# Performance work log

Measured on AMD Instinct MI355X. Metric: run time of the kernel, lower is better.

Reference implementation:

```python
import jax, jax.numpy as jnp
import numpy as np

HEADS = 4

def _unfold3x3(x):
    # x: [N, C, H, W] -> [N, C*9, H*W], channel-slowest / kernel-fastest (matches torch F.unfold)
    N, C, H, W = x.shape
    p = jnp.pad(x, ((0, 0), (0, 0), (1, 1), (1, 1)))
    pats = jnp.stack([p[:, :, i:i + H, j:j + W] for i in range(3) for j in range(3)], axis=2)
    return pats.reshape(N, C * 9, H * W)

def _conv1x1(x, w):
    # x: [N, Cin, H, W], w: [Cout, Cin]
    return jnp.einsum('nchw,oc->nohw', x, w)

def _dwconv3x3(x, w):
    # depthwise 3x3, x: [N, C, H, W], w: [C, 1, 3, 3]
    return jax.lax.conv_general_dilated(
        x, w, window_strides=(1, 1), padding='SAME',
        feature_group_count=x.shape[1],
        dimension_numbers=('NCHW', 'OIHW', 'NCHW'))

def _layernorm(x, w, b, eps=1e-5):
    m = jnp.mean(x, axis=-1, keepdims=True)
    v = jnp.mean(jnp.square(x - m), axis=-1, keepdims=True)
    return (x - m) * jax.lax.rsqrt(v + eps) * w + b

def _l2norm(x, eps=1e-12):
    n = jnp.sqrt(jnp.sum(jnp.square(x), axis=-1, keepdims=True))
    return x / jnp.maximum(n, eps)

def setup_inputs() -> dict:
    key = jax.random.key(0)
    ks = jax.random.split(key, 12)
    channels, angRes, h, w, b = 64, 5, 32, 32, 1
    a = angRes * angRes
    D = channels * 2          # 128
    hid = int(D * 2.66)       # 340
    s = 0.02
    return {
        'buffer': jax.random.normal(ks[0], (b, channels, a, h, w), jnp.float32),
        'mlp_w': jax.random.normal(ks[1], (D, channels * 9), jnp.float32) * s,
        'ln_attn_w': jnp.ones((D,), jnp.float32),
        'ln_attn_b': jnp.zeros((D,), jnp.float32),
        'ln_ffn_w': jnp.ones((D,), jnp.float32),
        'ln_ffn_b': jnp.zeros((D,), jnp.float32),
        'qkv_w': jax.random.normal(ks[2], (3 * D, D), jnp.float32) * s,
        'qkv_dw_w': jax.random.normal(ks[3], (3 * D, 1, 3, 3), jnp.float32) * s,
        'temperature': jnp.ones((HEADS, 1, 1), jnp.float32),
        'proj_attn_w': jax.random.normal(ks[4], (D, D), jnp.float32) * s,
        'ffn_in_w': jax.random.normal(ks[5], (2 * hid, D), jnp.float32) * s,
        'ffn_dw_w': jax.random.normal(ks[6], (2 * hid, 1, 3, 3), jnp.float32) * s,
        'ffn_out_w': jax.random.normal(ks[7], (D, hid), jnp.float32) * s,
        'proj3d_w': jax.random.normal(ks[8], (channels, D), jnp.float32) * s,
    }

def reference(buffer, mlp_w, ln_attn_w, ln_attn_b, ln_ffn_w, ln_ffn_b,
              qkv_w, qkv_dw_w, temperature, proj_attn_w,
              ffn_in_w, ffn_dw_w, ffn_out_w, proj3d_w):
    b, c, a, h, w = buffer.shape
    N, D = b * a, mlp_w.shape[0]
    L = h * w
    cph = D // HEADS

    # SAI2Token: [b,c,a,h,w] -> [(b a),c,h,w] -> unfold -> [L, N, c*9] -> MLP -> [L, N, D]
    buf2d = buffer.transpose(0, 2, 1, 3, 4).reshape(N, c, h, w)
    tok = _unfold3x3(buf2d).transpose(2, 0, 1)          # [L, N, c*9]
    tok = tok @ mlp_w.T                                  # [L, N, D]

    # --- attention branch ---
    tn = _layernorm(tok, ln_attn_w, ln_attn_b)
    x = tn.transpose(1, 2, 0).reshape(N, D, h, w)        # '(h w) n d -> n d h w'
    qkv = _dwconv3x3(_conv1x1(x, qkv_w), qkv_dw_w)       # [N, 3D, h, w]
    q, k, v = jnp.split(qkv, 3, axis=1)

    def heads(t):  # 'n (head c) h w -> n head (h w) c'
        return t.reshape(N, HEADS, cph, L).transpose(0, 1, 3, 2)
    q, k, v = heads(q), heads(k), heads(v)
    q, k = _l2norm(q), _l2norm(k)
    attn = jnp.einsum('nhlc,nhmc->nhlm', q, k) * temperature  # [N, HEADS, L, L]
    attn = jax.nn.softmax(attn, axis=-1)
    out = jnp.einsum('nhlm,nhmc->nhlc', attn, v)         # [N, HEADS, L, cph]
    out = out.transpose(0, 1, 3, 2).reshape(N, D, h, w)
    out = _conv1x1(out, proj_attn_w)
    tok = tok + out.reshape(N, D, L).transpose(2, 0, 1)

    # --- GDFN branch ---
    tf = _layernorm(tok, ln_ffn_w, ln_ffn_b)
    x2 = tf.transpose(1, 2, 0).reshape(N, D, h, w)
    y = _dwconv3x3(_conv1x1(x2, ffn_in_w), ffn_dw_w)     # [N, 2*hid, h, w]
    y1, y2 = jnp.split(y, 2, axis=1)
    y = jax.nn.gelu(y1, approximate=False) * y2
    y = _conv1x1(y, ffn_out_w)                           # [N, D, h, w]
    tok = tok + y.reshape(N, D, L).transpose(2, 0, 1)

    # Token2SAI: '(h w) (b a) d -> b d a h w' then 1x1x1 conv3d
    x5 = tok.reshape(h, w, b, a, D).transpose(2, 4, 3, 0, 1)  # [b, D, a, h, w]
    out = jnp.einsum('bdahw,od->boahw', x5, proj3d_w)
    return out
```

## Files before the change

### kernel.cpp

```cpp
#include <hip/hip_runtime.h>
#include <math.h>

#define M_TOK 25600

typedef __attribute__((ext_vector_type(8))) short bf16x8;
typedef __attribute__((ext_vector_type(4))) float f32x4;
typedef __attribute__((ext_vector_type(4))) int   i32x4;
typedef __attribute__((ext_vector_type(2))) int   i32x2;

__device__ __forceinline__ unsigned short f2b(float x) {
    unsigned u = __builtin_bit_cast(unsigned, x);
    return (unsigned short)((u + 0x7fffu + ((u >> 16) & 1u)) >> 16);
}
__device__ __forceinline__ float b2f(unsigned short h) {
    unsigned u = ((unsigned)h) << 16;
    return __builtin_bit_cast(float, u);
}
__device__ __forceinline__ unsigned cvtpk(float lo, float hi) {
    unsigned r;
    asm("v_cvt_pk_bf16_f32 %0, %1, %2" : "=v"(r) : "v"(lo), "v"(hi));
    return r;
}

__global__ __launch_bounds__(256) void prep_k(const float* __restrict__ s0, const float* __restrict__ s1,
                                              const float* __restrict__ s2, const float* __restrict__ s3,
                                              const float* __restrict__ s4, const float* __restrict__ s5,
                                              const float* __restrict__ qw, const float* __restrict__ fw,
                                              short* __restrict__ dst,
                                              float* __restrict__ wqT, float* __restrict__ wgT) {
    int i = blockIdx.x * 256 + threadIdx.x;
    if (i >= 297320) return;
    if (i < 287744) {
        if (i < 81920) {
            int r = i % 640, d = i / 640;
            int tap = r >> 6, cc = r & 63;
            dst[i] = (tap < 9) ? (short)f2b(s0[(d * 64 + cc) * 9 + tap]) : (short)0;
            return;
        }
        if (i >= 234496 && i < 279552) {
            int l = i - 234496;
            int row = l / 352, col = l % 352;
            dst[i] = (col < 340) ? (short)f2b(s4[row * 340 + col]) : (short)0;
            return;
        }
        const float* s; int off;
        if      (i < 131072) { s = s1; off = i - 81920; }
        else if (i < 147456) { s = s2; off = i - 131072; }
        else if (i < 234496) { s = s3; off = i - 147456; }
        else                 { s = s5; off = i - 279552; }
        dst[i] = (short)f2b(s[off]);
        return;
    }
    int j = i - 287744;
    if (j < 3456) {
        int tap = j / 384, c = j % 384;
        wqT[j] = qw[c * 9 + tap];
    } else {
        int k = j - 3456;
        int tap = k / 680, c = k % 680;
        wgT[k] = fw[c * 9 + tap];
    }
}

template <bool ADD, bool TROUT, bool AF32>
__global__ __launch_bounds__(256) void mm64_k(const void* __restrict__ Avp,
                                              const short* __restrict__ W,
                                              float* __restrict__ outp,
                                              int M, int N, int K) {
    __shared__ __align__(16) short As[2][64 * 40];
    __shared__ __align__(16) short Bs[2][64 * 40];
    const int tid = threadIdx.x;
    const int bm = blockIdx.x * 64;
    const int bn = blockIdx.y * 64;
    const int w = tid >> 6, lane = tid & 63;
    const int h = lane >> 4, l15 = lane & 15;
    const int wm = (w >> 1) * 32, wn = (w & 1) * 32;

    const int row = tid >> 2, c4 = tid & 3;
    const int gnW = bn + row;

    f32x4 acc[2][2];
#pragma unroll
    for (int i = 0; i < 2; ++i)
#pragma unroll
        for (int j = 0; j < 2; ++j) acc[i][j] = (f32x4){0.f, 0.f, 0.f, 0.f};

    short av[8], wv[8];

    auto ldA = [&](int k0, short* tmp) {
        int gk = k0 + c4 * 8;
        size_t abase = (size_t)(bm + row) * K + gk;
        if (AF32) {
            const float* ap = (const float*)Avp + abase;
            float4 va = *(const float4*)ap;
            float4 vb = *(const float4*)(ap + 4);
            tmp[0] = (short)f2b(va.x); tmp[1] = (short)f2b(va.y);
            tmp[2] = (short)f2b(va.z); tmp[3] = (short)f2b(va.w);
            tmp[4] = (short)f2b(vb.x); tmp[5] = (short)f2b(vb.y);
            tmp[6] = (short)f2b(vb.z); tmp[7] = (short)f2b(vb.w);
        } else {
            const short* ap = (const short*)Avp + abase;
            i32x2 a = *(const i32x2*)ap;
            i32x2 b = *(const i32x2*)(ap + 4);
            *(i32x2*)&tmp[0] = a; *(i32x2*)&tmp[4] = b;
        }
    };
    auto ldW = [&](int k0, short* tmp) {
        const short* wp = W + (size_t)gnW * K + k0 + c4 * 8;
        i32x2 a = *(const i32x2*)wp;
        i32x2 b = *(const i32x2*)(wp + 4);
        *(i32x2*)&tmp[0] = a; *(i32x2*)&tmp[4] = b;
    };

    ldA(0, av);
    ldW(0, wv);

    int ph = 0;
    for (int k0 = 0; k0 < K; k0 += 32, ph ^= 1) {
        *(i32x4*)&As[ph][row * 40 + c4 * 8] = *(i32x4*)av;
        *(i32x4*)&Bs[ph][row * 40 + c4 * 8] = *(i32x4*)wv;
        if (k0 + 32 < K) {
            ldA(k0 + 32, av);
            ldW(k0 + 32, wv);
        }
        __syncthreads();

        bf16x8 af[2], bf[2];
#pragma unroll
        for (int mi = 0; mi < 2; ++mi) af[mi] = *(const bf16x8*)&As[ph][(wm + mi * 16 + l15) * 40 + h * 8];
#pragma unroll
        for (int nj = 0; nj < 2; ++nj) bf[nj] = *(const bf16x8*)&Bs[ph][(wn + nj * 16 + l15) * 40 + h * 8];
#pragma unroll
        for (int mi = 0; mi < 2; ++mi)
#pragma unroll
            for (int nj = 0; nj < 2; ++nj) {
                if (TROUT)
                    acc[mi][nj] = __builtin_amdgcn_mfma_f32_16x16x32_bf16(bf[nj], af[mi], acc[mi][nj], 0, 0, 0);
                else
                    acc[mi][nj] = __builtin_amdgcn_mfma_f32_16x16x32_bf16(af[mi], bf[nj], acc[mi][nj], 0, 0, 0);
            }
    }

    if (!TROUT) {
#pragma unroll
        for (int mi = 0; mi < 2; ++mi) {
#pragma unroll
            for (int nj = 0; nj < 2; ++nj) {
                int gn = bn + wn + nj * 16 + l15;
#pragma unroll
                for (int r = 0; r < 4; ++r) {
                    int gm = bm + wm + mi * 16 + h * 4 + r;
                    size_t oi = (size_t)gm * N + gn;
                    if (ADD) outp[oi] += acc[mi][nj][r];
                    else     outp[oi] = acc[mi][nj][r];
                }
            }
        }
    } else {
#pragma unroll
        for (int mi = 0; mi < 2; ++mi) {
            int gm = bm + wm + mi * 16 + l15;
#pragma unroll
            for (int nj = 0; nj < 2; ++nj)
#pragma unroll
                for (int r = 0; r < 4; ++r) {
                    int gn = bn + wn + nj * 16 + h * 4 + r;
                    outp[(size_t)gn * M + gm] = acc[mi][nj][r];
                }
        }
    }
}

__global__ __launch_bounds__(256) void mmim_k(const float* __restrict__ buf,
                                              const short* __restrict__ W,
                                              float* __restrict__ outp) {
    const int N = 128, K = 640;
    __shared__ __align__(16) short As[2][128 * 40];
    __shared__ __align__(16) short Bs[2][64 * 40];
    const int tid = threadIdx.x;
    const int bm = blockIdx.x * 128;
    const int bn = blockIdx.y * 64;
    const int w = tid >> 6, lane = tid & 63;
    const int h = lane >> 4, l15 = lane & 15;
    const int wm = (w >> 1) * 64, wn = (w & 1) * 32;

    const int rowA0 = tid >> 2, c4 = tid & 3;
    const int rowA1 = rowA0 + 64;
    const int gnW = bn + rowA0;

    f32x4 acc[4][2];
#pragma unroll
    for (int i = 0; i < 4; ++i)
#pragma unroll
        for (int j = 0; j < 2; ++j) acc[i][j] = (f32x4){0.f, 0.f, 0.f, 0.f};

    auto ldA = [&](int row, int k0, short* tmp) {
        int t = bm + row;
        int l = t & 1023, n = t >> 10;
        int y = l >> 5, x = l & 31;
        int k = k0 + c4 * 8;
        int tap = k >> 6, cc0 = k & 63;
        bool ok = (tap < 9);
        int ti = 0, tj = 0;
        if (ok) { ti = tap / 3; tj = tap - ti * 3; }
        int yy = y + ti - 1, xx = x + tj - 1;
        ok = ok && (yy >= 0) && (yy < 32) && (xx >= 0) && (xx < 32);
        if (ok) {
            const float* bp = buf + (size_t)cc0 * M_TOK + (n << 10) + (yy << 5) + xx;
#pragma unroll
            for (int i = 0; i < 8; ++i) tmp[i] = (short)f2b(bp[(size_t)i * M_TOK]);
        } else {
#pragma unroll
            for (int i = 0; i < 8; ++i) tmp[i] = 0;
        }
    };
    auto ldW = [&](int k0, short* tmp) {
        const short* wp = W + (size_t)gnW * K + k0 + c4 * 8;
        i32x2 a = *(const i32x2*)wp;
        i32x2 b = *(const i32x2*)(wp + 4);
        *(i32x2*)&tmp[0] = a; *(i32x2*)&tmp[4] = b;
    };
    auto compute = [&](int ph) {
        bf16x8 af[4], bf[2];
#pragma unroll
        for (int mi = 0; mi < 4; ++mi) af[mi] = *(const bf16x8*)&As[ph][(wm + mi * 16 + l15) * 40 + h * 8];
#pragma unroll
        for (int nj = 0; nj < 2; ++nj) bf[nj] = *(const bf16x8*)&Bs[ph][(wn + nj * 16 + l15) * 40 + h * 8];
#pragma unroll
        for (int mi = 0; mi < 4; ++mi)
#pragma unroll
            for (int nj = 0; nj < 2; ++nj)
                acc[mi][nj] = __builtin_amdgcn_mfma_f32_16x16x32_bf16(af[mi], bf[nj], acc[mi][nj], 0, 0, 0);
    };

    short a0A[8], a1A[8], wvA[8];
    short a0B[8], a1B[8], wvB[8];
    ldA(rowA0, 0, a0A);  ldA(rowA1, 0, a1A);  ldW(0, wvA);
    ldA(rowA0, 32, a0B); ldA(rowA1, 32, a1B); ldW(32, wvB);

    for (int k0 = 0; k0 < K; k0 += 64) {
        *(i32x4*)&As[0][rowA0 * 40 + c4 * 8] = *(i32x4*)a0A;
        *(i32x4*)&As[0][rowA1 * 40 + c4 * 8] = *(i32x4*)a1A;
        *(i32x4*)&Bs[0][rowA0 * 40 + c4 * 8] = *(i32x4*)wvA;
        if (k0 + 64 < K) { ldA(rowA0, k0 + 64, a0A); ldA(rowA1, k0 + 64, a1A); ldW(k0 + 64, wvA); }
        __syncthreads();
        compute(0);
        *(i32x4*)&As[1][rowA0 * 40 + c4 * 8] = *(i32x4*)a0B;
        *(i32x4*)&As[1][rowA1 * 40 + c4 * 8] = *(i32x4*)a1B;
        *(i32x4*)&Bs[1][rowA0 * 40 + c4 * 8] = *(i32x4*)wvB;
        if (k0 + 96 < K) { ldA(rowA0, k0 + 96, a0B); ldA(rowA1, k0 + 96, a1B); ldW(k0 + 96, wvB); }
        __syncthreads();
        compute(1);
    }

#pragma unroll
    for (int mi = 0; mi < 4; ++mi) {
#pragma unroll
        for (int nj = 0; nj < 2; ++nj) {
            int gn = bn + wn + nj * 16 + l15;
#pragma unroll
            for (int r = 0; r < 4; ++r) {
                int gm = bm + wm + mi * 16 + h * 4 + r;
                outp[(size_t)gm * N + gn] = acc[mi][nj][r];
            }
        }
    }
}

__global__ __launch_bounds__(256) void mmw_k(const short* __restrict__ A,
                                             const short* __restrict__ W,
                                             short* __restrict__ outp,
                                             int M, int N, int K) {
    __shared__ __align__(16) short As[2][128 * 40];
    __shared__ __align__(16) short Bs[2][128 * 40];
    const int tid = threadIdx.x;
    const int bm = blockIdx.x * 128;
    const int bn = blockIdx.y * 128;
    const int w = tid >> 6, lane = tid & 63;
    const int h = lane >> 4, l15 = lane & 15;
    const int wm = (w >> 1) * 64, wn = (w & 1) * 64;

    const int row0 = tid >> 2, c4 = tid & 3;
    const int row1 = row0 + 64;

    f32x4 acc[4][4];
#pragma unroll
    for (int i = 0; i < 4; ++i)
#pragma unroll
        for (int j = 0; j < 4; ++j) acc[i][j] = (f32x4){0.f, 0.f, 0.f, 0.f};

    auto ldA = [&](int row, int k0, short* tmp) {
        const short* ap = A + (size_t)(bm + row) * K + k0 + c4 * 8;
        i32x2 x = *(const i32x2*)ap;
        i32x2 y = *(const i32x2*)(ap + 4);
        *(i32x2*)&tmp[0] = x; *(i32x2*)&tmp[4] = y;
    };
    auto ldW = [&](int row, int k0, short* tmp) {
        int gn = bn + row;
        if (gn < N) {
            const short* wp = W + (size_t)gn * K + k0 + c4 * 8;
            i32x2 x = *(const i32x2*)wp;
            i32x2 y = *(const i32x2*)(wp + 4);
            *(i32x2*)&tmp[0] = x; *(i32x2*)&tmp[4] = y;
        } else {
#pragma unroll
            for (int i = 0; i < 8; ++i) tmp[i] = 0;
        }
    };
    auto compute = [&](int ph) {
        bf16x8 af[4], bf[4];
#pragma unroll
        for (int mi = 0; mi < 4; ++mi) af[mi] = *(const bf16x8*)&As[ph][(wm + mi * 16 + l15) * 40 + h * 8];
#pragma unroll
        for (int nj = 0; nj < 4; ++nj) bf[nj] = *(const bf16x8*)&Bs[ph][(wn + nj * 16 + l15) * 40 + h * 8];
#pragma unroll
        for (int mi = 0; mi < 4; ++mi)
#pragma unroll
            for (int nj = 0; nj < 4; ++nj)
                acc[mi][nj] = __builtin_amdgcn_mfma_f32_16x16x32_bf16(af[mi], bf[nj], acc[mi][nj], 0, 0, 0);
    };

    short a0A[8], a1A[8], b0A[8], b1A[8];
    short a0B[8], a1B[8], b0B[8], b1B[8];
    ldA(row0, 0, a0A);  ldA(row1, 0, a1A);  ldW(row0, 0, b0A);  ldW(row1, 0, b1A);
    ldA(row0, 32, a0B); ldA(row1, 32, a1B); ldW(row0, 32, b0B); ldW(row1, 32, b1B);

    for (int k0 = 0; k0 < K; k0 += 64) {
        *(i32x4*)&As[0][row0 * 40 + c4 * 8] = *(i32x4*)a0A;
        *(i32x4*)&As[0][row1 * 40 + c4 * 8] = *(i32x4*)a1A;
        *(i32x4*)&Bs[0][row0 * 40 + c4 * 8] = *(i32x4*)b0A;
        *(i32x4*)&Bs[0][row1 * 40 + c4 * 8] = *(i32x4*)b1A;
        if (k0 + 64 < K) {
            ldA(row0, k0 + 64, a0A); ldA(row1, k0 + 64, a1A);
            ldW(row0, k0 + 64, b0A); ldW(row1, k0 + 64, b1A);
        }
        __syncthreads();
        compute(0);
        *(i32x4*)&As[1][row0 * 40 + c4 * 8] = *(i32x4*)a0B;
        *(i32x4*)&As[1][row1 * 40 + c4 * 8] = *(i32x4*)a1B;
        *(i32x4*)&Bs[1][row0 * 40 + c4 * 8] = *(i32x4*)b0B;
        *(i32x4*)&Bs[1][row1 * 40 + c4 * 8] = *(i32x4*)b1B;
        if (k0 + 96 < K) {
            ldA(row0, k0 + 96, a0B); ldA(row1, k0 + 96, a1B);
            ldW(row0, k0 + 96, b0B); ldW(row1, k0 + 96, b1B);
        }
        __syncthreads();
        compute(1);
    }

#pragma unroll
    for (int mi = 0; mi < 4; ++mi) {
#pragma unroll
        for (int nj = 0; nj < 4; ++nj) {
            int gn = bn + wn + nj * 16 + l15;
            if (gn < N) {
#pragma unroll
                for (int r = 0; r < 4; ++r) {
                    int gm = bm + wm + mi * 16 + h * 4 + r;
                    outp[(size_t)gm * N + gn] = (short)f2b(acc[mi][nj][r]);
                }
            }
        }
    }
}

__global__ __launch_bounds__(256) void ln_k(const float* __restrict__ in,
                                            const float* __restrict__ w,
                                            const float* __restrict__ b,
                                            short* __restrict__ out) {
    int t = blockIdx.x * 4 + (threadIdx.x >> 6);
    int lane = threadIdx.x & 63;
    float2 v = *(const float2*)(in + (size_t)t * 128 + lane * 2);
    float s = v.x + v.y, sq = v.x * v.x + v.y * v.y;
#pragma unroll
    for (int off = 32; off > 0; off >>= 1) { s += __shfl_xor(s, off); sq += __shfl_xor(sq, off); }
    float mean = s * (1.f / 128.f);
    float var = sq * (1.f / 128.f) - mean * mean;
    float rstd = rsqrtf(var + 1e-5f);
    float2 wv = *(const float2*)(w + lane * 2);
    float2 bv = *(const float2*)(b + lane * 2);
    float ox = (v.x - mean) * rstd * wv.x + bv.x;
    float oy = (v.y - mean) * rstd * wv.y + bv.y;
    ((unsigned*)out)[(size_t)t * 64 + lane] = f2b(ox) | ((unsigned)f2b(oy) << 16);
}

__global__ __launch_bounds__(256) void dwl2n_k(const short* __restrict__ in,
                                               const float* __restrict__ wqT,
                                               const float* __restrict__ temp,
                                               short* __restrict__ out) {
    int idx = blockIdx.x * 256 + threadIdx.x;
    int q = idx % 48;
    int t = idx / 48;
    int c0 = q * 8;
    int l = t & 1023, n = t >> 10;
    int y = l >> 5, x = l & 31;
    int tb = n << 10;

    float acc[8];
#pragma unroll
    for (int k = 0; k < 8; ++k) acc[k] = 0.f;

#pragma unroll
    for (int i = 0; i < 3; ++i) {
        int yy = y + i - 1;
        if (yy < 0 || yy >= 32) continue;
#pragma unroll
        for (int j = 0; j < 3; ++j) {
            int xx = x + j - 1;
            if (xx < 0 || xx >= 32) continue;
            bf16x8 d = *(const bf16x8*)(in + (size_t)(tb + (yy << 5) + xx) * 384 + c0);
            float4 wa = *(const float4*)(wqT + (i * 3 + j) * 384 + c0);
            float4 wb = *(const float4*)(wqT + (i * 3 + j) * 384 + c0 + 4);
            acc[0] += b2f((unsigned short)d[0]) * wa.x;
            acc[1] += b2f((unsigned short)d[1]) * wa.y;
            acc[2] += b2f((unsigned short)d[2]) * wa.z;
            acc[3] += b2f((unsigned short)d[3]) * wa.w;
            acc[4] += b2f((unsigned short)d[4]) * wb.x;
            acc[5] += b2f((unsigned short)d[5]) * wb.y;
            acc[6] += b2f((unsigned short)d[6]) * wb.z;
            acc[7] += b2f((unsigned short)d[7]) * wb.w;
        }
    }
    float ss = 0.f;
#pragma unroll
    for (int k = 0; k < 8; ++k) ss += acc[k] * acc[k];
    ss += __shfl_xor(ss, 1);
    ss += __shfl_xor(ss, 2);
    float sc;
    if (c0 < 128)       sc = (1.f / fmaxf(sqrtf(ss), 1e-12f)) * temp[c0 >> 5] * 1.44269504089f;
    else if (c0 < 256)  sc = 1.f / fmaxf(sqrtf(ss), 1e-12f);
    else                sc = 1.f;
    unsigned o[4];
#pragma unroll
    for (int k = 0; k < 4; ++k)
        o[k] = f2b(acc[2 * k] * sc) | ((unsigned)f2b(acc[2 * k + 1] * sc) << 16);
    *(i32x4*)(out + (size_t)t * 384 + c0) = *(i32x4*)o;
}

__global__ __launch_bounds__(256) void gdfn2_k(const short* __restrict__ in,
                                               const float* __restrict__ wgT,
                                               short* __restrict__ out) {
    int idx = blockIdx.x * 256 + threadIdx.x;
    int q = idx % 44;
    int t = idx / 44;
    int c0 = q * 8;
    short* op = out + (size_t)t * 352 + c0;
    if (q == 43) {
        *(i32x4*)op = (i32x4){0, 0, 0, 0};
        return;
    }
    int l = t & 1023, n = t >> 10;
    int y = l >> 5, x = l & 31;
    int tb = n << 10;

    float a[8], g[8];
#pragma unroll
    for (int k = 0; k < 8; ++k) { a[k] = 0.f; g[k] = 0.f; }

#pragma unroll
    for (int i = 0; i < 3; ++i) {
        int yy = y + i - 1;
        if (yy < 0 || yy >= 32) continue;
#pragma unroll
        for (int j = 0; j < 3; ++j) {
            int xx = x + j - 1;
            if (xx < 0 || xx >= 32) continue;
            const short* p = in + (size_t)(tb + (yy << 5) + xx) * 680 + c0;
            bf16x8 d1 = *(const bf16x8*)p;
            i32x2 d2a = *(const i32x2*)(p + 340);
            i32x2 d2b = *(const i32x2*)(p + 344);
            short d2[8];
            *(i32x2*)&d2[0] = d2a; *(i32x2*)&d2[4] = d2b;
            const float* wp = wgT + (i * 3 + j) * 680 + c0;
            float4 w1a = *(const float4*)wp;
            float4 w1b = *(const float4*)(wp + 4);
            float w1[8] = {w1a.x, w1a.y, w1a.z, w1a.w, w1b.x, w1b.y, w1b.z, w1b.w};
            float w2[8];
#pragma unroll
            for (int k = 0; k < 8; ++k) w2[k] = wp[340 + k];
#pragma unroll
            for (int k = 0; k < 8; ++k) {
                a[k] += b2f((unsigned short)d1[k]) * w1[k];
                g[k] += b2f((unsigned short)d2[k]) * w2[k];
            }
        }
    }
    unsigned o[4];
#pragma unroll
    for (int k = 0; k < 4; ++k) {
        float r0 = 0.5f * a[2 * k] * (1.f + erff(a[2 * k] * 0.70710678118f)) * g[2 * k];
        float r1 = 0.5f * a[2 * k + 1] * (1.f + erff(a[2 * k + 1] * 0.70710678118f)) * g[2 * k + 1];
        o[k] = f2b(r0) | ((unsigned)f2b(r1) << 16);
    }
    if (q == 42) { o[2] = 0; o[3] = 0; }
    *(i32x4*)op = *(i32x4*)o;
}

__global__ __launch_bounds__(256) void attn_k(const short* __restrict__ qkv,
                                              short* __restrict__ outp) {
    __shared__ __align__(16) short Ks[2][64 * 40];
    __shared__ __align__(16) short Vp[2][2048];
    const int b = blockIdx.x;
    const int orig = (b & 7) * 200 + (b >> 3);
    const int qt = orig & 15, nh = orig >> 4;
    const int hd = nh & 3, n = nh >> 2;
    const int tid = threadIdx.x;
    const int w = tid >> 6, lane = tid & 63;
    const int h = lane >> 4, l15 = lane & 15;
    const size_t base = (size_t)n * 1024 * 384;
    const int qrow = qt * 64 + w * 16 + l15;

    bf16x8 qf = *(const bf16x8*)(qkv + base + (size_t)qrow * 384 + hd * 32 + h * 8);
    f32x4 o0 = {0.f,0.f,0.f,0.f}, o1 = {0.f,0.f,0.f,0.f};
    f32x4 osum = {0.f,0.f,0.f,0.f};
    union { unsigned u[4]; bf16x8 v; } ones;
#pragma unroll
    for (int r = 0; r < 4; ++r) ones.u[r] = 0x3F803F80u;

    const int skey = tid >> 2, sc4 = tid & 3;
    const int sg = skey >> 5, skey5 = skey & 31;
    const int sh = (skey5 >> 2) & 3;
    const int sj = (skey5 & 3) + ((skey5 >> 4) << 2);
    const int sgran0 = (sg * 4 + sh) * 32 + sc4 * 8;
    const short* kbase = qkv + base + (size_t)skey * 384 + 128 + hd * 32 + sc4 * 8;

    auto scatterV = [&](int nb, i32x4 vreg) {
        short vs[8];
        *(i32x4*)vs = vreg;
#pragma unroll
        for (int i = 0; i < 8; ++i) {
            int gran = sgran0 + i;
            gran ^= (gran >> 3) & 7;
            Vp[nb][gran * 8 + sj] = vs[i];
        }
    };
    auto compute = [&](int nb) {
        const bf16x8 kf0 = *(const bf16x8*)&Ks[nb][l15 * 40 + h * 8];
        const bf16x8 kf1 = *(const bf16x8*)&Ks[nb][(16 + l15) * 40 + h * 8];
        const bf16x8 kf2 = *(const bf16x8*)&Ks[nb][(32 + l15) * 40 + h * 8];
        const bf16x8 kf3 = *(const bf16x8*)&Ks[nb][(48 + l15) * 40 + h * 8];
        int gr0 = h * 32 + l15;            gr0 ^= (gr0 >> 3) & 7;
        int gr1 = h * 32 + 16 + l15;       gr1 ^= (gr1 >> 3) & 7;
        int gr2 = (4 + h) * 32 + l15;      gr2 ^= (gr2 >> 3) & 7;
        int gr3 = (4 + h) * 32 + 16 + l15; gr3 ^= (gr3 >> 3) & 7;
        const bf16x8 va0 = *(const bf16x8*)&Vp[nb][gr0 * 8];
        const bf16x8 va1 = *(const bf16x8*)&Vp[nb][gr1 * 8];
        const bf16x8 vb0 = *(const bf16x8*)&Vp[nb][gr2 * 8];
        const bf16x8 vb1 = *(const bf16x8*)&Vp[nb][gr3 * 8];
        const f32x4 z = {0.f, 0.f, 0.f, 0.f};

        __builtin_amdgcn_s_setprio(1);
        f32x4 s0 = __builtin_amdgcn_mfma_f32_16x16x32_bf16(kf0, qf, z, 0, 0, 0);
        f32x4 s1 = __builtin_amdgcn_mfma_f32_16x16x32_bf16(kf1, qf, z, 0, 0, 0);
        f32x4 s2 = __builtin_amdgcn_mfma_f32_16x16x32_bf16(kf2, qf, z, 0, 0, 0);
        f32x4 s3 = __builtin_amdgcn_mfma_f32_16x16x32_bf16(kf3, qf, z, 0, 0, 0);
        __builtin_amdgcn_s_setprio(0);
        float p[16];
#pragma unroll
        for (int r = 0; r < 4; ++r) {
            p[r]      = exp2f(s0[r]);
            p[4 + r]  = exp2f(s1[r]);
            p[8 + r]  = exp2f(s2[r]);
            p[12 + r] = exp2f(s3[r]);
        }
        union { unsigned u[4]; bf16x8 v; } pf1, pf2;
#pragma unroll
        for (int r = 0; r < 4; ++r) {
            pf1.u[r] = cvtpk(p[2 * r], p[2 * r + 1]);
            pf2.u[r] = cvtpk(p[8 + 2 * r], p[8 + 2 * r + 1]);
        }
        __builtin_amdgcn_s_setprio(1);
        osum = __builtin_amdgcn_mfma_f32_16x16x32_bf16(ones.v, pf1.v, osum, 0, 0, 0);
        osum = __builtin_amdgcn_mfma_f32_16x16x32_bf16(ones.v, pf2.v, osum, 0, 0, 0);
        o0 = __builtin_amdgcn_mfma_f32_16x16x32_bf16(va0, pf1.v, o0, 0, 0, 0);
        o1 = __builtin_amdgcn_mfma_f32_16x16x32_bf16(va1, pf1.v, o1, 0, 0, 0);
        o0 = __builtin_amdgcn_mfma_f32_16x16x32_bf16(vb0, pf2.v, o0, 0, 0, 0);
        o1 = __builtin_amdgcn_mfma_f32_16x16x32_bf16(vb1, pf2.v, o1, 0, 0, 0);
        __builtin_amdgcn_s_setprio(0);
    };

    i32x4 kregA = *(const i32x4*)kbase;
    i32x4 vregA = *(const i32x4*)(kbase + 128);
    i32x4 kregB = *(const i32x4*)(kbase + (size_t)64 * 384);
    i32x4 vregB = *(const i32x4*)(kbase + (size_t)64 * 384 + 128);

    for (int t = 0; t < 16; t += 2) {
        *(i32x4*)&Ks[0][skey * 40 + sc4 * 8] = kregA;
        scatterV(0, vregA);
        if (t + 2 < 16) {
            const short* kp = kbase + (size_t)(t + 2) * 64 * 384;
            kregA = *(const i32x4*)kp;
            vregA = *(const i32x4*)(kp + 128);
        }
        __syncthreads();
        compute(0);
        *(i32x4*)&Ks[1][skey * 40 + sc4 * 8] = kregB;
        scatterV(1, vregB);
        if (t + 3 < 16) {
            const short* kp = kbase + (size_t)(t + 3) * 64 * 384;
            kregB = *(const i32x4*)kp;
            vregB = *(const i32x4*)(kp + 128);
        }
        __syncthreads();
        compute(1);
    }

    float inv = 1.f / osum[0];

    size_t ob = ((size_t)n * 1024 + qrow) * 128 + hd * 32;
    unsigned u;
    u = f2b(o0[0] * inv) | ((unsigned)f2b(o0[1] * inv) << 16); *(unsigned*)(outp + ob + h * 4) = u;
    u = f2b(o0[2] * inv) | ((unsigned)f2b(o0[3] * inv) << 16); *(unsigned*)(outp + ob + h * 4 + 2) = u;
    u = f2b(o1[0] * inv) | ((unsigned)f2b(o1[1] * inv) << 16); *(unsigned*)(outp + ob + 16 + h * 4) = u;
    u = f2b(o1[2] * inv) | ((unsigned)f2b(o1[3] * inv) << 16); *(unsigned*)(outp + ob + 16 + h * 4 + 2) = u;
}

extern "C" void kernel_launch(void* const* d_in, const int* in_sizes, int n_in,
                              void* d_out, int out_size, void* d_ws, size_t ws_size,
                              hipStream_t stream) {
    const float* buffer      = (const float*)d_in[0];
    const float* mlp_w       = (const float*)d_in[1];
    const float* ln_attn_w   = (const float*)d_in[2];
    const float* ln_attn_b   = (const float*)d_in[3];
    const float* ln_ffn_w    = (const float*)d_in[4];
    const float* ln_ffn_b    = (const float*)d_in[5];
    const float* qkv_w       = (const float*)d_in[6];
    const float* qkv_dw_w    = (const float*)d_in[7];
    const float* temperature = (const float*)d_in[8];
    const float* proj_attn_w = (const float*)d_in[9];
    const float* ffn_in_w    = (const float*)d_in[10];
    const float* ffn_dw_w    = (const float*)d_in[11];
    const float* ffn_out_w   = (const float*)d_in[12];
    const float* proj3d_w    = (const float*)d_in[13];

    char* wsb = (char*)d_ws;
    short* Wbf     = (short*)wsb;
    short* mlpW    = Wbf;
    short* qkvW    = Wbf + 81920;
    short* projW   = Wbf + 131072;
    short* ffnInW  = Wbf + 147456;
    short* ffnOutW = Wbf + 234496;
    short* p3dW    = Wbf + 279552;
    float* wqT     = (float*)(wsb + 575488);
    float* wgT     = (float*)(wsb + 589312);
    float* tok     = (float*)(wsb + 33381792);
    short* LNbf    = (short*)(wsb + 46488992);
    short* QKVpre  = (short*)(wsb + 53042592);
    short* qkvb    = (short*)(wsb + 72703392);
    short* AObf    = (short*)(wsb + 92364192);
    short* F1      = (short*)(wsb + 98917792);
    short* G       = (short*)(wsb + 133733792);

    dim3 blk(256);

    prep_k<<<1162, blk, 0, stream>>>(mlp_w, qkv_w, proj_attn_w, ffn_in_w, ffn_out_w, proj3d_w,
                                     qkv_dw_w, ffn_dw_w, Wbf, wqT, wgT);

    mmim_k<<<dim3(200, 2), blk, 0, stream>>>(buffer, mlpW, tok);
    ln_k<<<6400, blk, 0, stream>>>(tok, ln_attn_w, ln_attn_b, LNbf);
    mmw_k<<<dim3(200, 3), blk, 0, stream>>>(LNbf, qkvW, QKVpre, M_TOK, 384, 128);
    dwl2n_k<<<4800, blk, 0, stream>>>(QKVpre, wqT, temperature, qkvb);
    attn_k<<<1600, blk, 0, stream>>>(qkvb, AObf);
    mm64_k<true, false, false><<<dim3(400, 2), blk, 0, stream>>>(AObf, projW, tok, M_TOK, 128, 128);
    ln_k<<<6400, blk, 0, stream>>>(tok, ln_ffn_w, ln_ffn_b, LNbf);
    mmw_k<<<dim3(200, 6), blk, 0, stream>>>(LNbf, ffnInW, F1, M_TOK, 680, 128);
    gdfn2_k<<<4400, blk, 0, stream>>>(F1, wgT, G);
    mm64_k<true, false, false><<<dim3(400, 2), blk, 0, stream>>>(G, ffnOutW, tok, M_TOK, 128, 352);
    mm64_k<false, true, true><<<dim3(400, 1), blk, 0, stream>>>(tok, p3dW, (float*)d_out, M_TOK, 64, 128);
}
```

Baseline: 201.4 us.

## Fuse LayerNorm into the im2col MLP GEMM and the attention projection GEMM

Both LayerNorm passes become GEMM epilogues. The im2col MLP GEMM and the attention projection GEMM now cover all 128 output channels in one block of 64 rows, so each row's mean and variance can be reduced in registers and shared memory. Each writes the fp32 residual token and the bf16 normalized output directly, which removes two standalone LN launches and their re-read of tok. In exchange the tiles are reshaped to 64x128, which changes A/B reuse and occupancy, and the variance uses the one-pass E[x^2]-mean^2 form.

```diff
diff --git a/kernel.cpp b/kernel.cpp
--- a/kernel.cpp
+++ b/kernel.cpp
@@ -171,31 +171,34 @@
     }
 }
 
-__global__ __launch_bounds__(256) void mmim_k(const float* __restrict__ buf,
-                                              const short* __restrict__ W,
-                                              float* __restrict__ outp) {
-    const int N = 128, K = 640;
-    __shared__ __align__(16) short As[2][128 * 40];
-    __shared__ __align__(16) short Bs[2][64 * 40];
+__global__ __launch_bounds__(256) void mmim_ln_k(const float* __restrict__ buf,
+                                                 const short* __restrict__ W,
+                                                 const float* __restrict__ lnw,
+                                                 const float* __restrict__ lnb,
+                                                 float* __restrict__ tok,
+                                                 short* __restrict__ lnout) {
+    const int K = 640;
+    __shared__ __align__(16) short As[2][64 * 40];
+    __shared__ __align__(16) short Bs[2][128 * 40];
+    __shared__ float lnbuf[64][2][2];
     const int tid = threadIdx.x;
-    const int bm = blockIdx.x * 128;
-    const int bn = blockIdx.y * 64;
+    const int bm = blockIdx.x * 64;
     const int w = tid >> 6, lane = tid & 63;
     const int h = lane >> 4, l15 = lane & 15;
-    const int wm = (w >> 1) * 64, wn = (w & 1) * 32;
-
-    const int rowA0 = tid >> 2, c4 = tid & 3;
-    const int rowA1 = rowA0 + 64;
-    const int gnW = bn + rowA0;
-
-    f32x4 acc[4][2];
-#pragma unroll
-    for (int i = 0; i < 4; ++i)
-#pragma unroll
-        for (int j = 0; j < 2; ++j) acc[i][j] = (f32x4){0.f, 0.f, 0.f, 0.f};
-
-    auto ldA = [&](int row, int k0, short* tmp) {
-        int t = bm + row;
+    const int wr = w >> 1, wc = w & 1;
+    const int wm = wr * 32, wn = wc * 64;
+
+    const int rowA = tid >> 2, c4 = tid & 3;
+    const int rowB1 = rowA + 64;
+
+    f32x4 acc[2][4];
+#pragma unroll
+    for (int i = 0; i < 2; ++i)
+#pragma unroll
+        for (int j = 0; j < 4; ++j) acc[i][j] = (f32x4){0.f, 0.f, 0.f, 0.f};
+
+    auto ldA = [&](int k0, short* tmp) {
+        int t = bm + rowA;
         int l = t & 1023, n = t >> 10;
         int y = l >> 5, x = l & 31;
         int k = k0 + c4 * 8;
@@ -214,57 +217,229 @@
             for (int i = 0; i < 8; ++i) tmp[i] = 0;
         }
     };
-    auto ldW = [&](int k0, short* tmp) {
-        const short* wp = W + (size_t)gnW * K + k0 + c4 * 8;
+    auto ldW = [&](int row, int k0, short* tmp) {
+        const short* wp = W + (size_t)row * K + k0 + c4 * 8;
         i32x2 a = *(const i32x2*)wp;
         i32x2 b = *(const i32x2*)(wp + 4);
         *(i32x2*)&tmp[0] = a; *(i32x2*)&tmp[4] = b;
     };
     auto compute = [&](int ph) {
-        bf16x8 af[4], bf[2];
-#pragma unroll
-        for (int mi = 0; mi < 4; ++mi) af[mi] = *(const bf16x8*)&As[ph][(wm + mi * 16 + l15) * 40 + h * 8];
-#pragma unroll
-        for (int nj = 0; nj < 2; ++nj) bf[nj] = *(const bf16x8*)&Bs[ph][(wn + nj * 16 + l15) * 40 + h * 8];
-#pragma unroll
-        for (int mi = 0; mi < 4; ++mi)
-#pragma unroll
-            for (int nj = 0; nj < 2; ++nj)
+        bf16x8 af[2], bf[4];
+#pragma unroll
+        for (int mi = 0; mi < 2; ++mi) af[mi] = *(const bf16x8*)&As[ph][(wm + mi * 16 + l15) * 40 + h * 8];
+#pragma unroll
+        for (int nj = 0; nj < 4; ++nj) bf[nj] = *(const bf16x8*)&Bs[ph][(wn + nj * 16 + l15) * 40 + h * 8];
+#pragma unroll
+        for (int mi = 0; mi < 2; ++mi)
+#pragma unroll
+            for (int nj = 0; nj < 4; ++nj)
                 acc[mi][nj] = __builtin_amdgcn_mfma_f32_16x16x32_bf16(af[mi], bf[nj], acc[mi][nj], 0, 0, 0);
     };
 
-    short a0A[8], a1A[8], wvA[8];
-    short a0B[8], a1B[8], wvB[8];
-    ldA(rowA0, 0, a0A);  ldA(rowA1, 0, a1A);  ldW(0, wvA);
-    ldA(rowA0, 32, a0B); ldA(rowA1, 32, a1B); ldW(32, wvB);
+    short aA[8], b0A[8], b1A[8];
+    short aB[8], b0B[8], b1B[8];
+    ldA(0, aA);  ldW(rowA, 0, b0A);  ldW(rowB1, 0, b1A);
+    ldA(32, aB); ldW(rowA, 32, b0B); ldW(rowB1, 32, b1B);
 
     for (int k0 = 0; k0 < K; k0 += 64) {
-        *(i32x4*)&As[0][rowA0 * 40 + c4 * 8] = *(i32x4*)a0A;
-        *(i32x4*)&As[0][rowA1 * 40 + c4 * 8] = *(i32x4*)a1A;
-        *(i32x4*)&Bs[0][rowA0 * 40 + c4 * 8] = *(i32x4*)wvA;
-        if (k0 + 64 < K) { ldA(rowA0, k0 + 64, a0A); ldA(rowA1, k0 + 64, a1A); ldW(k0 + 64, wvA); }
+        *(i32x4*)&As[0][rowA * 40 + c4 * 8]  = *(i32x4*)aA;
+        *(i32x4*)&Bs[0][rowA * 40 + c4 * 8]  = *(i32x4*)b0A;
+        *(i32x4*)&Bs[0][rowB1 * 40 + c4 * 8] = *(i32x4*)b1A;
+        if (k0 + 64 < K) { ldA(k0 + 64, aA); ldW(rowA, k0 + 64, b0A); ldW(rowB1, k0 + 64, b1A); }
         __syncthreads();
         compute(0);
-        *(i32x4*)&As[1][rowA0 * 40 + c4 * 8] = *(i32x4*)a0B;
-        *(i32x4*)&As[1][rowA1 * 40 + c4 * 8] = *(i32x4*)a1B;
-        *(i32x4*)&Bs[1][rowA0 * 40 + c4 * 8] = *(i32x4*)wvB;
-        if (k0 + 96 < K) { ldA(rowA0, k0 + 96, a0B); ldA(rowA1, k0 + 96, a1B); ldW(k0 + 96, wvB); }
+        *(i32x4*)&As[1][rowA * 40 + c4 * 8]  = *(i32x4*)aB;
+        *(i32x4*)&Bs[1][rowA * 40 + c4 * 8]  = *(i32x4*)b0B;
+        *(i32x4*)&Bs[1][rowB1 * 40 + c4 * 8] = *(i32x4*)b1B;
+        if (k0 + 96 < K) { ldA(k0 + 96, aB); ldW(rowA, k0 + 96, b0B); ldW(rowB1, k0 + 96, b1B); }
         __syncthreads();
         compute(1);
     }
 
 #pragma unroll
-    for (int mi = 0; mi < 4; ++mi) {
-#pragma unroll
-        for (int nj = 0; nj < 2; ++nj) {
-            int gn = bn + wn + nj * 16 + l15;
-#pragma unroll
-            for (int r = 0; r < 4; ++r) {
-                int gm = bm + wm + mi * 16 + h * 4 + r;
-                outp[(size_t)gm * N + gn] = acc[mi][nj][r];
-            }
-        }
-    }
+    for (int mi = 0; mi < 2; ++mi)
+#pragma unroll
+        for (int rr = 0; rr < 4; ++rr) {
+            float s = 0.f, q = 0.f;
+#pragma unroll
+            for (int nj = 0; nj < 4; ++nj) {
+                float v = acc[mi][nj][rr];
+                s += v; q += v * v;
+            }
+#pragma unroll
+            for (int off = 1; off < 16; off <<= 1) {
+                s += __shfl_xor(s, off);
+                q += __shfl_xor(q, off);
+            }
+            if (l15 == 0) {
+                int rl = wm + mi * 16 + h * 4 + rr;
+                lnbuf[rl][wc][0] = s;
+                lnbuf[rl][wc][1] = q;
+            }
+        }
+    __syncthreads();
+
+    float wl[4], bl[4];
+#pragma unroll
+    for (int nj = 0; nj < 4; ++nj) {
+        int gn = wn + nj * 16 + l15;
+        wl[nj] = lnw[gn];
+        bl[nj] = lnb[gn];
+    }
+#pragma unroll
+    for (int mi = 0; mi < 2; ++mi)
+#pragma unroll
+        for (int rr = 0; rr < 4; ++rr) {
+            int rl = wm + mi * 16 + h * 4 + rr;
+            int gm = bm + rl;
+            float S = lnbuf[rl][0][0] + lnbuf[rl][1][0];
+            float Q = lnbuf[rl][0][1] + lnbuf[rl][1][1];
+            float mean = S * (1.f / 128.f);
+            float var = Q * (1.f / 128.f) - mean * mean;
+            float rstd = rsqrtf(var + 1e-5f);
+#pragma unroll
+            for (int nj = 0; nj < 4; ++nj) {
+                int gn = wn + nj * 16 + l15;
+                float v = acc[mi][nj][rr];
+                tok[(size_t)gm * 128 + gn] = v;
+                float o = (v - mean) * rstd * wl[nj] + bl[nj];
+                lnout[(size_t)gm * 128 + gn] = (short)f2b(o);
+            }
+        }
+}
+
+__global__ __launch_bounds__(256) void pmln_k(const short* __restrict__ A,
+                                              const short* __restrict__ W,
+                                              const float* __restrict__ lnw,
+                                              const float* __restrict__ lnb,
+                                              float* __restrict__ tok,
+                                              short* __restrict__ lnout) {
+    const int K = 128;
+    __shared__ __align__(16) short As[2][64 * 40];
+    __shared__ __align__(16) short Bs[2][128 * 40];
+    __shared__ float lnbuf[64][2][2];
+    const int tid = threadIdx.x;
+    const int bm = blockIdx.x * 64;
+    const int w = tid >> 6, lane = tid & 63;
+    const int h = lane >> 4, l15 = lane & 15;
+    const int wr = w >> 1, wc = w & 1;
+    const int wm = wr * 32, wn = wc * 64;
+
+    const int rowA = tid >> 2, c4 = tid & 3;
+    const int rowB1 = rowA + 64;
+
+    f32x4 acc[2][4];
+#pragma unroll
+    for (int i = 0; i < 2; ++i)
+#pragma unroll
+        for (int j = 0; j < 4; ++j) acc[i][j] = (f32x4){0.f, 0.f, 0.f, 0.f};
+
+    auto ldA = [&](int k0, short* tmp) {
+        const short* ap = A + (size_t)(bm + rowA) * K + k0 + c4 * 8;
+        i32x2 a = *(const i32x2*)ap;
+        i32x2 b = *(const i32x2*)(ap + 4);
+        *(i32x2*)&tmp[0] = a; *(i32x2*)&tmp[4] = b;
+    };
+    auto ldW = [&](int row, int k0, short* tmp) {
+        const short* wp = W + (size_t)row * K + k0 + c4 * 8;
+        i32x2 a = *(const i32x2*)wp;
+        i32x2 b = *(const i32x2*)(wp + 4);
+        *(i32x2*)&tmp[0] = a; *(i32x2*)&tmp[4] = b;
+    };
+    auto compute = [&](int ph) {
+        bf16x8 af[2], bf[4];
+#pragma unroll
+        for (int mi = 0; mi < 2; ++mi) af[mi] = *(const bf16x8*)&As[ph][(wm + mi * 16 + l15) * 40 + h * 8];
+#pragma unroll
+        for (int nj = 0; nj < 4; ++nj) bf[nj] = *(const bf16x8*)&Bs[ph][(wn + nj * 16 + l15) * 40 + h * 8];
+#pragma unroll
+        for (int mi = 0; mi < 2; ++mi)
+#pragma unroll
+            for (int nj = 0; nj < 4; ++nj)
+                acc[mi][nj] = __builtin_amdgcn_mfma_f32_16x16x32_bf16(af[mi], bf[nj], acc[mi][nj], 0, 0, 0);
+    };
+
+    short aA[8], b0A[8], b1A[8];
+    short aB[8], b0B[8], b1B[8];
+    ldA(0, aA);  ldW(rowA, 0, b0A);  ldW(rowB1, 0, b1A);
+    ldA(32, aB); ldW(rowA, 32, b0B); ldW(rowB1, 32, b1B);
+
+    for (int k0 = 0; k0 < K; k0 += 64) {
+        *(i32x4*)&As[0][rowA * 40 + c4 * 8]  = *(i32x4*)aA;
+        *(i32x4*)&Bs[0][rowA * 40 + c4 * 8]  = *(i32x4*)b0A;
+        *(i32x4*)&Bs[0][rowB1 * 40 + c4 * 8] = *(i32x4*)b1A;
+        if (k0 + 64 < K) { ldA(k0 + 64, aA); ldW(rowA, k0 + 64, b0A); ldW(rowB1, k0 + 64, b1A); }
+        __syncthreads();
+        compute(0);
+        *(i32x4*)&As[1][rowA * 40 + c4 * 8]  = *(i32x4*)aB;
+        *(i32x4*)&Bs[1][rowA * 40 + c4 * 8]  = *(i32x4*)b0B;
+        *(i32x4*)&Bs[1][rowB1 * 40 + c4 * 8] = *(i32x4*)b1B;
+        if (k0 + 96 < K) { ldA(k0 + 96, aB); ldW(rowA, k0 + 96, b0B); ldW(rowB1, k0 + 96, b1B); }
+        __syncthreads();
+        compute(1);
+    }
+
+#pragma unroll
+    for (int mi = 0; mi < 2; ++mi)
+#pragma unroll
+        for (int rr = 0; rr < 4; ++rr) {
+            int gm = bm + wm + mi * 16 + h * 4 + rr;
+#pragma unroll
+            for (int nj = 0; nj < 4; ++nj) {
+                int gn = wn + nj * 16 + l15;
+                acc[mi][nj][rr] += tok[(size_t)gm * 128 + gn];
+            }
+        }
+#pragma unroll
+    for (int mi = 0; mi < 2; ++mi)
+#pragma unroll
+        for (int rr = 0; rr < 4; ++rr) {
+            float s = 0.f, q = 0.f;
+#pragma unroll
+            for (int nj = 0; nj < 4; ++nj) {
+                float v = acc[mi][nj][rr];
+                s += v; q += v * v;
+            }
+#pragma unroll
+            for (int off = 1; off < 16; off <<= 1) {
+                s += __shfl_xor(s, off);
+                q += __shfl_xor(q, off);
+            }
+            if (l15 == 0) {
+                int rl = wm + mi * 16 + h * 4 + rr;
+                lnbuf[rl][wc][0] = s;
+                lnbuf[rl][wc][1] = q;
+            }
+        }
+    __syncthreads();
+
+    float wl[4], bl[4];
+#pragma unroll
+    for (int nj = 0; nj < 4; ++nj) {
+        int gn = wn + nj * 16 + l15;
+        wl[nj] = lnw[gn];
+        bl[nj] = lnb[gn];
+    }
+#pragma unroll
+    for (int mi = 0; mi < 2; ++mi)
+#pragma unroll
+        for (int rr = 0; rr < 4; ++rr) {
+            int rl = wm + mi * 16 + h * 4 + rr;
+            int gm = bm + rl;
+            float S = lnbuf[rl][0][0] + lnbuf[rl][1][0];
+            float Q = lnbuf[rl][0][1] + lnbuf[rl][1][1];
+            float mean = S * (1.f / 128.f);
+            float var = Q * (1.f / 128.f) - mean * mean;
+            float rstd = rsqrtf(var + 1e-5f);
+#pragma unroll
+            for (int nj = 0; nj < 4; ++nj) {
+                int gn = wn + nj * 16 + l15;
+                float v = acc[mi][nj][rr];
+                tok[(size_t)gm * 128 + gn] = v;
+                float o = (v - mean) * rstd * wl[nj] + bl[nj];
+                lnout[(size_t)gm * 128 + gn] = (short)f2b(o);
+            }
+        }
 }
 
 __global__ __launch_bounds__(256) void mmw_k(const short* __restrict__ A,
@@ -362,26 +537,6 @@
             }
         }
     }
-}
-
-__global__ __launch_bounds__(256) void ln_k(const float* __restrict__ in,
-                                            const float* __restrict__ w,
-                                            const float* __restrict__ b,
-                                            short* __restrict__ out) {
-    int t = blockIdx.x * 4 + (threadIdx.x >> 6);
-    int lane = threadIdx.x & 63;
-    float2 v = *(const float2*)(in + (size_t)t * 128 + lane * 2);
-    float s = v.x + v.y, sq = v.x * v.x + v.y * v.y;
-#pragma unroll
-    for (int off = 32; off > 0; off >>= 1) { s += __shfl_xor(s, off); sq += __shfl_xor(sq, off); }
-    float mean = s * (1.f / 128.f);
-    float var = sq * (1.f / 128.f) - mean * mean;
-    float rstd = rsqrtf(var + 1e-5f);
-    float2 wv = *(const float2*)(w + lane * 2);
-    float2 bv = *(const float2*)(b + lane * 2);
-    float ox = (v.x - mean) * rstd * wv.x + bv.x;
-    float oy = (v.y - mean) * rstd * wv.y + bv.y;
-    ((unsigned*)out)[(size_t)t * 64 + lane] = f2b(ox) | ((unsigned)f2b(oy) << 16);
 }
 
 __global__ __launch_bounds__(256) void dwl2n_k(const short* __restrict__ in,
@@ -656,13 +811,11 @@
     prep_k<<<1162, blk, 0, stream>>>(mlp_w, qkv_w, proj_attn_w, ffn_in_w, ffn_out_w, proj3d_w,
                                      qkv_dw_w, ffn_dw_w, Wbf, wqT, wgT);
 
-    mmim_k<<<dim3(200, 2), blk, 0, stream>>>(buffer, mlpW, tok);
-    ln_k<<<6400, blk, 0, stream>>>(tok, ln_attn_w, ln_attn_b, LNbf);
+    mmim_ln_k<<<400, blk, 0, stream>>>(buffer, mlpW, ln_attn_w, ln_attn_b, tok, LNbf);
     mmw_k<<<dim3(200, 3), blk, 0, stream>>>(LNbf, qkvW, QKVpre, M_TOK, 384, 128);
     dwl2n_k<<<4800, blk, 0, stream>>>(QKVpre, wqT, temperature, qkvb);
     attn_k<<<1600, blk, 0, stream>>>(qkvb, AObf);
-    mm64_k<true, false, false><<<dim3(400, 2), blk, 0, stream>>>(AObf, projW, tok, M_TOK, 128, 128);
-    ln_k<<<6400, blk, 0, stream>>>(tok, ln_ffn_w, ln_ffn_b, LNbf);
+    pmln_k<<<400, blk, 0, stream>>>(AObf, projW, ln_ffn_w, ln_ffn_b, tok, LNbf);
     mmw_k<<<dim3(200, 6), blk, 0, stream>>>(LNbf, ffnInW, F1, M_TOK, 680, 128);
     gdfn2_k<<<4400, blk, 0, stream>>>(F1, wgT, G);
     mm64_k<true, false, false><<<dim3(400, 2), blk, 0, stream>>>(G, ffnOutW, tok, M_TOK, 128, 352);
```

New measurement: 183.5 us. 8.9% less time.
